# Kernel tuning notes

Measured on AMD Instinct MI355X. Metric: run time of the kernel, lower is better.

Reference implementation:

```python
import jax, jax.numpy as jnp
import numpy as np

EPS = 1e-5

def conv1x1(x, w, b):
    # x: [B,Cin,H,W], w: [Cout,Cin], b: [Cout]
    return jnp.einsum('oi,bihw->bohw', w, x) + b[None, :, None, None]

def self_attention(x, qw, qb, kw, kb, vw, vb, fw, fb):
    B, C, H, W = x.shape
    hid = qw.shape[0]
    q = conv1x1(x, qw, qb).reshape(B, hid, H * W).transpose(0, 2, 1)   # [B,HW,hid]
    k = conv1x1(x, kw, kb).reshape(B, hid, H * W)                      # [B,hid,HW]
    v = conv1x1(x, vw, vb).reshape(B, C, H * W)                        # [B,C,HW]
    attn = jax.nn.softmax(jnp.einsum('bnh,bhm->bnm', q, k), axis=-1)   # [B,HW,HW]
    z = jnp.einsum('bnm,bcm->bnc', attn, v)                            # [B,HW,C]
    # faithful to torch .view(B,C,H,W) on contiguous [B,HW,C]: raw reshape, no transpose
    z = z.reshape(B, C, H, W)
    return conv1x1(z * x, fw, fb) + x

def group_norm_per_channel(y, gw, gb):
    # GroupNorm(num_groups == num_channels): per-channel instance norm, biased var
    mean = y.mean(axis=(2, 3), keepdims=True)
    var = ((y - mean) ** 2).mean(axis=(2, 3), keepdims=True)
    yn = (y - mean) * jax.lax.rsqrt(var + EPS)
    return yn * gw[None, :, None, None] + gb[None, :, None, None]

def setup_inputs() -> dict:
    key = jax.random.key(0)
    ks = jax.random.split(key, 32)
    B, C, H, W = 4, 64, 64, 64
    hid, att = 64, 64
    d = {}
    d['x'] = jax.random.normal(ks[0], (B, C, H, W), jnp.float32)
    d['h'] = jax.random.normal(ks[1], (B, hid, H, W), jnp.float32)
    d['c'] = jax.random.normal(ks[2], (B, hid, H, W), jnp.float32)
    i = 3
    for pre, cin in (('ax', C), ('ah', hid)):
        for nm, cout in (('q', att), ('k', att), ('v', cin), ('f', cin)):
            d[f'{pre}_{nm}w'] = jax.random.normal(ks[i], (cout, cin), jnp.float32) * 0.05; i += 1
            d[f'{pre}_{nm}b'] = jax.random.normal(ks[i], (cout,), jnp.float32) * 0.05; i += 1
    d['conv_w'] = jax.random.normal(ks[i], (4 * hid, C + hid, 3, 3), jnp.float32) * 0.05; i += 1
    d['conv_b'] = jax.random.normal(ks[i], (4 * hid,), jnp.float32) * 0.05; i += 1
    d['gn_w'] = jnp.ones((4 * hid,), jnp.float32)
    d['gn_b'] = jnp.zeros((4 * hid,), jnp.float32)
    return d

def reference(x, h, c,
              ax_qw, ax_qb, ax_kw, ax_kb, ax_vw, ax_vb, ax_fw, ax_fb,
              ah_qw, ah_qb, ah_kw, ah_kb, ah_vw, ah_vb, ah_fw, ah_fb,
              conv_w, conv_b, gn_w, gn_b):
    hid = h.shape[1]
    xa = self_attention(x, ax_qw, ax_qb, ax_kw, ax_kb, ax_vw, ax_vb, ax_fw, ax_fb)
    ha = self_attention(h, ah_qw, ah_qb, ah_kw, ah_kb, ah_vw, ah_vb, ah_fw, ah_fb)
    combined = jnp.concatenate([xa, ha], axis=1)
    y = jax.lax.conv_general_dilated(
        combined, conv_w, window_strides=(1, 1), padding=[(1, 1), (1, 1)],
        dimension_numbers=('NCHW', 'OIHW', 'NCHW')) + conv_b[None, :, None, None]
    y = group_norm_per_channel(y, gn_w, gn_b)
    i, f, o, g = jnp.split(y, 4, axis=1)
    i = jax.nn.sigmoid(i); f = jax.nn.sigmoid(f); o = jax.nn.sigmoid(o); g = jnp.tanh(g)
    c_next = f * c + i * g
    h_next = o * jnp.tanh(c_next)
    return jnp.stack([h_next, c_next])  # [2,B,hid,H,W]
```

## Files before the change

kernel.cpp:

```cpp
#include <hip/hip_runtime.h>
#include <hip/hip_bf16.h>


typedef __hip_bfloat16 bf16;
typedef const __hip_bfloat16* bfp;
typedef short bf16x8 __attribute__((ext_vector_type(8)));
typedef short short4v __attribute__((ext_vector_type(4)));
typedef float f32x4 __attribute__((ext_vector_type(4)));

#define SM_SHIFT 12.0f

__device__ __forceinline__ float ldf(const void* p, long i, int f32) {
    return f32 ? ((const float*)p)[i]
               : __bfloat162float(((const bf16*)p)[i]);
}
__device__ __forceinline__ short f2bf(float f) {
    bf16 h = __float2bfloat16(f);
    return *reinterpret_cast<short*>(&h);
}

__global__ void sniff_kernel(const void* __restrict__ x, int* __restrict__ flag)
{
    const unsigned short* u = (const unsigned short*)x;
    int lane = threadIdx.x;
    int ok = 0;
    for (int i = 0; i < 4; ++i) {
        int e = (u[lane * 4 + i] >> 7) & 0xFF;
        ok += (e >= 100 && e <= 141);
    }
    ok += __shfl_xor(ok, 1, 64);
    ok += __shfl_xor(ok, 2, 64);
    ok += __shfl_xor(ok, 4, 64);
    ok += __shfl_xor(ok, 8, 64);
    ok += __shfl_xor(ok, 16, 64);
    ok += __shfl_xor(ok, 32, 64);
    if (lane == 0) *flag = (ok < 200) ? 1 : 0;
}

__global__ __launch_bounds__(256) void wt_kernel(
    const void* __restrict__ cw, bf16* __restrict__ Wt,
    float* __restrict__ gacc, const int* __restrict__ flag)
{
    if (blockIdx.x == 0) {
        for (int j = 0; j < 8; ++j)
            gacc[threadIdx.x * 8 + j] = 0.f;
    }
    int f32 = *flag;
    int idx = blockIdx.x * 256 + threadIdx.x;
    int tap = idx >> 15;
    int rem = idx & 32767;
    int oc = rem >> 7, ic = rem & 127;
    Wt[idx] = __float2bfloat16(ldf(cw, ((long)oc * 128 + ic) * 9 + tap, f32));
}

__global__ __launch_bounds__(256) void qkv_kernel(
    const void* __restrict__ Xx, const void* __restrict__ Xh,
    const void* __restrict__ qwx, const void* __restrict__ qbx,
    const void* __restrict__ kwx, const void* __restrict__ kbx,
    const void* __restrict__ vwx, const void* __restrict__ vbx,
    const void* __restrict__ qwh, const void* __restrict__ qbh,
    const void* __restrict__ kwh, const void* __restrict__ kbh,
    const void* __restrict__ vwh, const void* __restrict__ vbh,
    bf16* __restrict__ Qx, bf16* __restrict__ Kx, bf16* __restrict__ Vtx,
    bf16* __restrict__ Qh, bf16* __restrict__ Kh, bf16* __restrict__ Vth,
    const int* __restrict__ flag)
{
    __shared__ __align__(16) short xt[64][72];
    __shared__ __align__(16) short wq[64][72];
    __shared__ __align__(16) short wk[64][72];
    __shared__ __align__(16) short wv[64][72];
    int ab  = blockIdx.x >> 8;
    int idx = blockIdx.x & 255;
    int b = idx >> 6;
    int n0 = (idx & 63) * 64;
    int tid = threadIdx.x;
    int wave = tid >> 6, lane = tid & 63;
    int q = lane >> 4, l15 = lane & 15;
    int f32 = *flag;

    const void* X = ab ? Xh : Xx;
    const void* qw = ab ? qwh : qwx; const void* qb = ab ? qbh : qbx;
    const void* kw = ab ? kwh : kwx; const void* kb = ab ? kbh : kbx;
    const void* vw = ab ? vwh : vwx; const void* vb = ab ? vbh : vbx;
    short* Qg  = (short*)(ab ? Qh  : Qx)  + (long)b * 262144;
    short* Kg  = (short*)(ab ? Kh  : Kx)  + (long)b * 262144;
    short* Vtg = (short*)(ab ? Vth : Vtx) + (long)b * 262144;

    if (!f32) {
        const short* q16 = (const short*)qw;
        const short* k16 = (const short*)kw;
        const short* v16 = (const short*)vw;
        for (int rep = 0; rep < 2; ++rep) {
            int j8 = (rep * 256 + tid) * 8;
            *(bf16x8*)&wq[j8 >> 6][j8 & 63] = *(const bf16x8*)(q16 + j8);
            *(bf16x8*)&wk[j8 >> 6][j8 & 63] = *(const bf16x8*)(k16 + j8);
            *(bf16x8*)&wv[j8 >> 6][j8 & 63] = *(const bf16x8*)(v16 + j8);
        }
    } else {
        for (int rep = 0; rep < 16; ++rep) {
            int j = rep * 256 + tid;
            int i = j >> 6, cc = j & 63;
            wq[i][cc] = f2bf(((const float*)qw)[j]);
            wk[i][cc] = f2bf(((const float*)kw)[j]);
            wv[i][cc] = f2bf(((const float*)vw)[j]);
        }
    }
    long xbase = (long)b * 262144;
    for (int rep = 0; rep < 16; ++rep) {
        int c = rep * 4 + (tid >> 6);
        int p = tid & 63;
        xt[p][c] = f2bf(ldf(X, xbase + (long)c * 4096 + n0 + p, f32));
    }
    __syncthreads();

    bf16x8 a0 = *(const bf16x8*)&xt[wave * 16 + l15][q * 8];
    bf16x8 a1 = *(const bf16x8*)&xt[wave * 16 + l15][32 + q * 8];

    for (int ct = 0; ct < 4; ++ct) {
        bf16x8 bq0 = *(const bf16x8*)&wq[ct * 16 + l15][q * 8];
        bf16x8 bq1 = *(const bf16x8*)&wq[ct * 16 + l15][32 + q * 8];
        f32x4 z = (f32x4){0.f, 0.f, 0.f, 0.f};
        z = __builtin_amdgcn_mfma_f32_16x16x32_bf16(a0, bq0, z, 0, 0, 0);
        z = __builtin_amdgcn_mfma_f32_16x16x32_bf16(a1, bq1, z, 0, 0, 0);
        float bias = ldf(qb, ct * 16 + l15, f32);
        for (int reg = 0; reg < 4; ++reg)
            Qg[(long)(n0 + wave * 16 + q * 4 + reg) * 64 + ct * 16 + l15] =
                f2bf(z[reg] + bias);
    }
    for (int ct = 0; ct < 4; ++ct) {
        bf16x8 bk0 = *(const bf16x8*)&wk[ct * 16 + l15][q * 8];
        bf16x8 bk1 = *(const bf16x8*)&wk[ct * 16 + l15][32 + q * 8];
        f32x4 z = (f32x4){0.f, 0.f, 0.f, 0.f};
        z = __builtin_amdgcn_mfma_f32_16x16x32_bf16(a0, bk0, z, 0, 0, 0);
        z = __builtin_amdgcn_mfma_f32_16x16x32_bf16(a1, bk1, z, 0, 0, 0);
        float bias = ldf(kb, ct * 16 + l15, f32);
        for (int reg = 0; reg < 4; ++reg)
            Kg[(long)(n0 + wave * 16 + q * 4 + reg) * 64 + ct * 16 + l15] =
                f2bf(z[reg] + bias);
    }
    bf16x8 av0 = *(const bf16x8*)&wv[wave * 16 + l15][q * 8];
    bf16x8 av1 = *(const bf16x8*)&wv[wave * 16 + l15][32 + q * 8];
    for (int ct = 0; ct < 4; ++ct) {
        bf16x8 bx0 = *(const bf16x8*)&xt[ct * 16 + l15][q * 8];
        bf16x8 bx1 = *(const bf16x8*)&xt[ct * 16 + l15][32 + q * 8];
        f32x4 z = (f32x4){0.f, 0.f, 0.f, 0.f};
        z = __builtin_amdgcn_mfma_f32_16x16x32_bf16(av0, bx0, z, 0, 0, 0);
        z = __builtin_amdgcn_mfma_f32_16x16x32_bf16(av1, bx1, z, 0, 0, 0);
        for (int reg = 0; reg < 4; ++reg) {
            int c_out = wave * 16 + q * 4 + reg;
            float bias = ldf(vb, c_out, f32);
            Vtg[(long)c_out * 4096 + n0 + ct * 16 + l15] = f2bf(z[reg] + bias);
        }
    }
}

__global__ __launch_bounds__(256, 2) void attn_kernel(
    bfp Qx, bfp Kx, bfp Vtx, bf16* Ox,
    bfp Qh, bfp Kh, bfp Vth, bf16* Oh)
{
    __shared__ __align__(16) short ks [2][64][64];
    __shared__ __align__(16) short vts[2][64][64];
    __shared__ __align__(16) short ps[4][16][64];
    int tid = threadIdx.x;
    int wave = tid >> 6, lane = tid & 63;
    int q = lane >> 4, l15 = lane & 15;
    int ab  = blockIdx.x >> 8;
    int idx = blockIdx.x & 255;
    int b = idx >> 6;
    int rt = idx & 63;
    int n0 = rt * 64 + wave * 16;
    const short* Qb  = (const short*)(ab ? Qh  : Qx)  + (long)b * 262144;
    const short* Kb  = (const short*)(ab ? Kh  : Kx)  + (long)b * 262144;
    const short* Vtb = (const short*)(ab ? Vth : Vtx) + (long)b * 262144;
    short* Ob = (short*)(ab ? Oh : Ox) + (long)b * 262144;

    bf16x8 aq0 = *(const bf16x8*)(Qb + (long)(n0 + l15) * 64 + q * 8);
    bf16x8 aq1 = *(const bf16x8*)(Qb + (long)(n0 + l15) * 64 + 32 + q * 8);

    f32x4 acc_o[4];
    for (int ct = 0; ct < 4; ++ct) acc_o[ct] = (f32x4){0.f, 0.f, 0.f, 0.f};
    float l_part[4] = {0.f, 0.f, 0.f, 0.f};

    int swp = (l15 >> 1) & 7;
    int c0 = (q ^ swp) << 3;
    int c1 = ((q + 4) ^ swp) << 3;
    int sw_s = (tid >> 4) & 7;
    int cs = (((tid & 7) ^ sw_s)) << 3;

    int r0 = tid >> 3, r1 = r0 + 32;
    bf16x8 pk0 = *(const bf16x8*)(Kb + (long)r0 * 64 + (tid & 7) * 8);
    bf16x8 pk1 = *(const bf16x8*)(Kb + (long)r1 * 64 + (tid & 7) * 8);
    bf16x8 pv0 = *(const bf16x8*)(Vtb + (long)r0 * 4096 + (tid & 7) * 8);
    bf16x8 pv1 = *(const bf16x8*)(Vtb + (long)r1 * 4096 + (tid & 7) * 8);

    for (int it = 0; it < 64; ++it) {
        int buf = it & 1;
        *(bf16x8*)&ks[buf][r0][cs]  = pk0;
        *(bf16x8*)&ks[buf][r1][cs]  = pk1;
        *(bf16x8*)&vts[buf][r0][cs] = pv0;
        *(bf16x8*)&vts[buf][r1][cs] = pv1;
        __syncthreads();
        if (it + 1 < 64) {
            long m = (long)(it + 1) * 64;
            pk0 = *(const bf16x8*)(Kb + (m + r0) * 64 + (tid & 7) * 8);
            pk1 = *(const bf16x8*)(Kb + (m + r1) * 64 + (tid & 7) * 8);
            pv0 = *(const bf16x8*)(Vtb + (long)r0 * 4096 + m + (tid & 7) * 8);
            pv1 = *(const bf16x8*)(Vtb + (long)r1 * 4096 + m + (tid & 7) * 8);
        }

        f32x4 s[4];
        for (int t = 0; t < 4; ++t) {
            const short* krow = &ks[buf][t * 16 + l15][0];
            bf16x8 bk0 = *(const bf16x8*)(krow + c0);
            bf16x8 bk1 = *(const bf16x8*)(krow + c1);
            f32x4 z = (f32x4){0.f, 0.f, 0.f, 0.f};
            z    = __builtin_amdgcn_mfma_f32_16x16x32_bf16(aq0, bk0, z, 0, 0, 0);
            s[t] = __builtin_amdgcn_mfma_f32_16x16x32_bf16(aq1, bk1, z, 0, 0, 0);
        }

        for (int t = 0; t < 4; ++t) {
            int chunkbase = t << 1 | (l15 >> 3);
            for (int reg = 0; reg < 4; ++reg) {
                float p = __expf(fminf(s[t][reg] - SM_SHIFT, 60.f));
                l_part[reg] += p;
                int n = q * 4 + reg;
                int swn = (n >> 1) & 7;
                ps[wave][n][((chunkbase ^ swn) << 3) | (l15 & 7)] = f2bf(p);
            }
        }

        const short* prow = &ps[wave][l15][0];
        bf16x8 bp0 = *(const bf16x8*)(prow + c0);
        bf16x8 bp1 = *(const bf16x8*)(prow + c1);
        for (int ct = 0; ct < 4; ++ct) {
            const short* vrow = &vts[buf][ct * 16 + l15][0];
            bf16x8 av0 = *(const bf16x8*)(vrow + c0);
            bf16x8 av1 = *(const bf16x8*)(vrow + c1);
            acc_o[ct] = __builtin_amdgcn_mfma_f32_16x16x32_bf16(av0, bp0, acc_o[ct], 0, 0, 0);
            acc_o[ct] = __builtin_amdgcn_mfma_f32_16x16x32_bf16(av1, bp1, acc_o[ct], 0, 0, 0);
        }
    }

    for (int reg = 0; reg < 4; ++reg) {
        l_part[reg] += __shfl_xor(l_part[reg], 1, 64);
        l_part[reg] += __shfl_xor(l_part[reg], 2, 64);
        l_part[reg] += __shfl_xor(l_part[reg], 4, 64);
        l_part[reg] += __shfl_xor(l_part[reg], 8, 64);
    }
    int src = (l15 >> 2) << 4;
    float L0 = __shfl(l_part[0], src, 64);
    float L1 = __shfl(l_part[1], src, 64);
    float L2 = __shfl(l_part[2], src, 64);
    float L3 = __shfl(l_part[3], src, 64);
    int r3 = l15 & 3;
    float ln = (r3 == 0) ? L0 : (r3 == 1) ? L1 : (r3 == 2) ? L2 : L3;
    float iln = 1.f / ln;
    for (int ct = 0; ct < 4; ++ct) {
        short o0 = f2bf(acc_o[ct][0] * iln);
        short o1 = f2bf(acc_o[ct][1] * iln);
        short o2 = f2bf(acc_o[ct][2] * iln);
        short o3 = f2bf(acc_o[ct][3] * iln);
        short* dst = Ob + (long)(n0 + l15) * 64 + ct * 16 + q * 4;
        dst[0] = o0; dst[1] = o1; dst[2] = o2; dst[3] = o3;
    }
}

__global__ __launch_bounds__(256) void attnout_kernel(
    bfp Ox, const void* __restrict__ Xx,
    const void* __restrict__ fwx, const void* __restrict__ fbx,
    bf16* __restrict__ outx,
    bfp Oh, const void* __restrict__ Xh,
    const void* __restrict__ fwh, const void* __restrict__ fbh,
    bf16* __restrict__ outh,
    const int* __restrict__ flag)
{
    __shared__ __align__(16) short fwt[64][72];
    __shared__ __align__(16) short at [64][72];
    int f32 = *flag;
    int ab  = blockIdx.x >> 8;
    int idx = blockIdx.x & 255;
    int b = idx >> 6;
    int h = idx & 63;
    int tid = threadIdx.x;
    int wave = tid >> 6, lane = tid & 63;
    int q = lane >> 4, l15 = lane & 15;
    bfp O = ab ? Oh : Ox;
    const void* X = ab ? Xh : Xx;
    const void* fw = ab ? fwh : fwx;
    const void* fb = ab ? fbh : fbx;
    bf16* out = ab ? outh : outx;

    if (!f32) {
        const short* f16p = (const short*)fw;
        for (int rep = 0; rep < 2; ++rep) {
            int j8 = (rep * 256 + tid) * 8;
            *(bf16x8*)&fwt[j8 >> 6][j8 & 63] = *(const bf16x8*)(f16p + j8);
        }
    } else {
        for (int rep = 0; rep < 16; ++rep) {
            int j = rep * 256 + tid;
            fwt[j >> 6][j & 63] = f2bf(((const float*)fw)[j]);
        }
    }
    const bf16* Ob = O + (long)b * 262144;
    long xbase = (long)b * 262144;
    {
        int w = tid & 63;
        for (int rep = 0; rep < 16; ++rep) {
            int cn = rep * 4 + (tid >> 6);
            float prod = __bfloat162float(Ob[(cn * 64 + h) * 64 + w]) *
                         ldf(X, xbase + (long)cn * 4096 + h * 64 + w, f32);
            at[w][cn] = f2bf(prod);
        }
    }
    __syncthreads();
    bf16x8 a0 = *(const bf16x8*)&fwt[wave * 16 + l15][q * 8];
    bf16x8 a1 = *(const bf16x8*)&fwt[wave * 16 + l15][32 + q * 8];
    short* outp = (short*)out;
    for (int nt = 0; nt < 4; ++nt) {
        bf16x8 b0 = *(const bf16x8*)&at[nt * 16 + l15][q * 8];
        bf16x8 b1 = *(const bf16x8*)&at[nt * 16 + l15][32 + q * 8];
        f32x4 z = (f32x4){0.f, 0.f, 0.f, 0.f};
        z = __builtin_amdgcn_mfma_f32_16x16x32_bf16(a0, b0, z, 0, 0, 0);
        z = __builtin_amdgcn_mfma_f32_16x16x32_bf16(a1, b1, z, 0, 0, 0);
        int w = nt * 16 + l15;
        short4v o4;
        for (int reg = 0; reg < 4; ++reg) {
            int o = wave * 16 + q * 4 + reg;
            float v = z[reg] + ldf(fb, o, f32) +
                      ldf(X, xbase + (long)o * 4096 + h * 64 + w, f32);
            o4[reg] = f2bf(v);
        }
        *(short4v*)(outp + (((long)(b * 64 + h) * 64 + w) * 64 + wave * 16 + q * 4)) = o4;
    }
}

__global__ __launch_bounds__(256) void conv3x3_kernel(
    bfp xa, bfp ha, bfp Wt, const void* __restrict__ cb,
    bf16* __restrict__ y, float* __restrict__ gacc,
    const int* __restrict__ flag)
{
    __shared__ __align__(16) short in_s[3][66][136];
    int f32 = *flag;
    int b = blockIdx.x >> 6;
    int h = blockIdx.x & 63;
    int tid = threadIdx.x;
    int wave = tid >> 6, lane = tid & 63;
    int q = lane >> 4, l15 = lane & 15;

    const short* xab = (const short*)xa + (long)b * 262144;
    const short* hab = (const short*)ha + (long)b * 262144;
    const bf16x8 zv = {0, 0, 0, 0, 0, 0, 0, 0};
    for (int r = 0; r < 3; ++r) {
        int gy = h + r - 1;
        bool valid = (gy >= 0) && (gy < 64);
        for (int s = 0; s < 2; ++s) {
            int strip = s * 256 + tid;
            int w = strip >> 3;
            int c8 = (strip & 7) * 8;
            bf16x8 vx = zv, vh = zv;
            if (valid) {
                vx = *(const bf16x8*)(xab + ((long)gy * 64 + w) * 64 + c8);
                vh = *(const bf16x8*)(hab + ((long)gy * 64 + w) * 64 + c8);
            }
            *(bf16x8*)&in_s[r][w + 1][c8]      = vx;
            *(bf16x8*)&in_s[r][w + 1][64 + c8] = vh;
        }
    }
    if (tid < 96) {
        int r = tid / 32;
        int rest = tid % 32;
        int col = (rest & 1) ? 65 : 0;
        int c8 = (rest >> 1) * 8;
        *(bf16x8*)&in_s[r][col][c8] = zv;
    }
    __syncthreads();

    int oc0 = wave * 64;
    f32x4 acc[4][4];
    for (int mt = 0; mt < 4; ++mt)
        for (int nt = 0; nt < 4; ++nt)
            acc[mt][nt] = (f32x4){0.f, 0.f, 0.f, 0.f};

    const short* Wb = (const short*)Wt;
    for (int tap = 0; tap < 9; ++tap) {
        int dy = tap / 3, dx = tap - dy * 3;
        for (int kc = 0; kc < 4; ++kc) {
            bf16x8 afrag[4];
            for (int mt = 0; mt < 4; ++mt)
                afrag[mt] = *(const bf16x8*)(
                    Wb + ((long)tap * 256 + oc0 + mt * 16 + l15) * 128 + kc * 32 + q * 8);
            for (int nt = 0; nt < 4; ++nt) {
                bf16x8 bfrag = *(const bf16x8*)&in_s[dy][nt * 16 + l15 + dx][kc * 32 + q * 8];
                for (int mt = 0; mt < 4; ++mt)
                    acc[mt][nt] = __builtin_amdgcn_mfma_f32_16x16x32_bf16(
                        afrag[mt], bfrag, acc[mt][nt], 0, 0, 0);
            }
        }
    }

    long ybase = (long)b * 1048576 + (long)h * 64;
    for (int mt = 0; mt < 4; ++mt) {
        for (int reg = 0; reg < 4; ++reg) {
            int oc = oc0 + mt * 16 + q * 4 + reg;
            float bias = ldf(cb, oc, f32);
            float s = 0.f, s2 = 0.f;
            for (int nt = 0; nt < 4; ++nt) {
                float v = acc[mt][nt][reg] + bias;
                ((short*)y)[ybase + (long)oc * 4096 + nt * 16 + l15] = f2bf(v);
                s += v; s2 = fmaf(v, v, s2);
            }
            s  += __shfl_xor(s,  1, 64);  s2 += __shfl_xor(s2, 1, 64);
            s  += __shfl_xor(s,  2, 64);  s2 += __shfl_xor(s2, 2, 64);
            s  += __shfl_xor(s,  4, 64);  s2 += __shfl_xor(s2, 4, 64);
            s  += __shfl_xor(s,  8, 64);  s2 += __shfl_xor(s2, 8, 64);
            if (l15 == 0) {
                atomicAdd(&gacc[b * 256 + oc], s);
                atomicAdd(&gacc[1024 + b * 256 + oc], s2);
            }
        }
    }
}

__global__ __launch_bounds__(256) void gates_kernel(
    bfp y, const float* __restrict__ gacc,
    const void* __restrict__ gw, const void* __restrict__ gb,
    const void* __restrict__ c_in, void* __restrict__ out,
    const int* __restrict__ flag)
{
    int f32 = *flag;
    int idx = blockIdx.x * 256 + threadIdx.x;
    int b = idx >> 18;
    int r = idx & 262143;
    int ch = r >> 12;
    int pix = r & 4095;
    long ybase = (long)b * 1048576;
    float vals[4];
    for (int g = 0; g < 4; ++g) {
        int cc = g * 64 + ch;
        float mu  = gacc[b * 256 + cc] * (1.f / 4096.f);
        float var = gacc[1024 + b * 256 + cc] * (1.f / 4096.f) - mu * mu;
        float rstd = rsqrtf(fmaxf(var, 0.f) + 1e-5f);
        float v = __bfloat162float(y[ybase + (long)cc * 4096 + pix]);
        v = (v - mu) * rstd * ldf(gw, cc, f32) + ldf(gb, cc, f32);
        vals[g] = v;
    }
    float ig = 1.f / (1.f + __expf(-vals[0]));
    float fg = 1.f / (1.f + __expf(-vals[1]));
    float og = 1.f / (1.f + __expf(-vals[2]));
    float gg = tanhf(vals[3]);
    float cprev = ldf(c_in, idx, f32);
    float cn = fg * cprev + ig * gg;
    float hn = og * tanhf(cn);
    if (f32) {
        float* o32 = (float*)out;
        o32[idx] = hn;
        o32[1048576 + idx] = cn;
    } else {
        bf16* o16 = (bf16*)out;
        o16[idx] = __float2bfloat16(hn);
        o16[1048576 + idx] = __float2bfloat16(cn);
    }
}

extern "C" void kernel_launch(void* const* d_in, const int* in_sizes, int n_in,
                              void* d_out, int out_size, void* d_ws, size_t ws_size,
                              hipStream_t stream)
{
    const void* x = d_in[0]; const void* h = d_in[1]; const void* c = d_in[2];
    const void* ax_qw = d_in[3],  *ax_qb = d_in[4];
    const void* ax_kw = d_in[5],  *ax_kb = d_in[6];
    const void* ax_vw = d_in[7],  *ax_vb = d_in[8];
    const void* ax_fw = d_in[9],  *ax_fb = d_in[10];
    const void* ah_qw = d_in[11], *ah_qb = d_in[12];
    const void* ah_kw = d_in[13], *ah_kb = d_in[14];
    const void* ah_vw = d_in[15], *ah_vb = d_in[16];
    const void* ah_fw = d_in[17], *ah_fb = d_in[18];
    const void* conv_w = d_in[19], *conv_b = d_in[20];
    const void* gn_w = d_in[21],  *gn_b = d_in[22];

    char* wsb = (char*)d_ws;
    auto S = [&](int i) { return wsb + ((unsigned long)i << 21); };
    bool fused = ws_size >= (18ul << 20) + 16384;

    bf16* ha = (bf16*)S(0);
    bf16* Wt = (bf16*)S(1);
    bf16 *Qx, *Kx, *Vtx, *Qh, *Kh, *Vth, *xa, *y;
    char* tail;
    if (fused) {
        Qx = (bf16*)S(2); Kx = (bf16*)S(3); Vtx = (bf16*)S(4);
        Qh = (bf16*)S(5); Kh = (bf16*)S(6); Vth = (bf16*)S(7);
        xa = (bf16*)S(8); y = Qx;
        tail = S(9);
    } else {
        Qx = (bf16*)S(2); Kx = (bf16*)S(3); Vtx = (bf16*)S(4);
        Qh = Qx; Kh = Kx; Vth = Vtx;
        xa = (bf16*)S(6); y = Qx;
        tail = S(7);
    }
    bf16* Ox = Qx;
    bf16* Oh = Qh;
    int*  flag = (int*)tail;
    float* gacc = (float*)(tail + 256);

    sniff_kernel<<<1, 64, 0, stream>>>(x, flag);

    if (fused) {
        qkv_kernel<<<512, 256, 0, stream>>>(
            x, h,
            ax_qw, ax_qb, ax_kw, ax_kb, ax_vw, ax_vb,
            ah_qw, ah_qb, ah_kw, ah_kb, ah_vw, ah_vb,
            Qx, Kx, Vtx, Qh, Kh, Vth, flag);
        attn_kernel<<<512, 256, 0, stream>>>(Qx, Kx, Vtx, Ox, Qh, Kh, Vth, Oh);
        attnout_kernel<<<512, 256, 0, stream>>>(
            Ox, x, ax_fw, ax_fb, xa, Oh, h, ah_fw, ah_fb, ha, flag);
    } else {
        qkv_kernel<<<256, 256, 0, stream>>>(
            x, x,
            ax_qw, ax_qb, ax_kw, ax_kb, ax_vw, ax_vb,
            ax_qw, ax_qb, ax_kw, ax_kb, ax_vw, ax_vb,
            Qx, Kx, Vtx, Qx, Kx, Vtx, flag);
        attn_kernel<<<256, 256, 0, stream>>>(Qx, Kx, Vtx, Ox, Qx, Kx, Vtx, Ox);
        attnout_kernel<<<256, 256, 0, stream>>>(
            Ox, x, ax_fw, ax_fb, xa, Ox, x, ax_fw, ax_fb, xa, flag);
        qkv_kernel<<<256, 256, 0, stream>>>(
            h, h,
            ah_qw, ah_qb, ah_kw, ah_kb, ah_vw, ah_vb,
            ah_qw, ah_qb, ah_kw, ah_kb, ah_vw, ah_vb,
            Qh, Kh, Vth, Qh, Kh, Vth, flag);
        attn_kernel<<<256, 256, 0, stream>>>(Qh, Kh, Vth, Oh, Qh, Kh, Vth, Oh);
        attnout_kernel<<<256, 256, 0, stream>>>(
            Oh, h, ah_fw, ah_fb, ha, Oh, h, ah_fw, ah_fb, ha, flag);
    }
    wt_kernel<<<1152, 256, 0, stream>>>(conv_w, Wt, gacc, flag);
    conv3x3_kernel<<<256, 256, 0, stream>>>(xa, ha, Wt, conv_b, y, gacc, flag);
    gates_kernel<<<4096, 256, 0, stream>>>(y, gacc, gn_w, gn_b, c, d_out, flag);
}
```

Measured before the change: 244.0 us.

## Split attention key dimension in two halves and combine partials in attnout

Attention blocks now process only half of the key/value sequence each, doubling the grid from 512 to 1024 blocks to fill more of the CUs. Each half writes unnormalized bf16 partial outputs and per-row softmax sums to workspace. The attnout kernel adds the two partials and normalizes them, which is possible because the softmax uses a fixed shift. This costs extra partial-output traffic, rounds the partials to bf16 before they are summed, and only runs when the workspace is at least 27 MB.

Result: no change. 239.4 us (-1.9%).

```diff
diff --git a/kernel.cpp b/kernel.cpp
--- a/kernel.cpp
+++ b/kernel.cpp
@@ -156,7 +156,8 @@
 
 __global__ __launch_bounds__(256, 2) void attn_kernel(
     bfp Qx, bfp Kx, bfp Vtx, bf16* Ox,
-    bfp Qh, bfp Kh, bfp Vth, bf16* Oh)
+    bfp Qh, bfp Kh, bfp Vth, bf16* Oh,
+    float* __restrict__ lw, int split)
 {
     __shared__ __align__(16) short ks [2][64][64];
     __shared__ __align__(16) short vts[2][64][64];
@@ -164,15 +165,21 @@
     int tid = threadIdx.x;
     int wave = tid >> 6, lane = tid & 63;
     int q = lane >> 4, l15 = lane & 15;
-    int ab  = blockIdx.x >> 8;
     int idx = blockIdx.x & 255;
+    int ab, half, mstart, ntile;
+    if (split) {
+        ab = blockIdx.x >> 9; half = (blockIdx.x >> 8) & 1;
+        mstart = half * 2048; ntile = 32;
+    } else {
+        ab = blockIdx.x >> 8; half = 0; mstart = 0; ntile = 64;
+    }
     int b = idx >> 6;
     int rt = idx & 63;
     int n0 = rt * 64 + wave * 16;
     const short* Qb  = (const short*)(ab ? Qh  : Qx)  + (long)b * 262144;
     const short* Kb  = (const short*)(ab ? Kh  : Kx)  + (long)b * 262144;
     const short* Vtb = (const short*)(ab ? Vth : Vtx) + (long)b * 262144;
-    short* Ob = (short*)(ab ? Oh : Ox) + (long)b * 262144;
+    short* Ob = (short*)(ab ? Oh : Ox) + (long)half * (1l << 20) + (long)b * 262144;
 
     bf16x8 aq0 = *(const bf16x8*)(Qb + (long)(n0 + l15) * 64 + q * 8);
     bf16x8 aq1 = *(const bf16x8*)(Qb + (long)(n0 + l15) * 64 + 32 + q * 8);
@@ -188,20 +195,20 @@
     int cs = (((tid & 7) ^ sw_s)) << 3;
 
     int r0 = tid >> 3, r1 = r0 + 32;
-    bf16x8 pk0 = *(const bf16x8*)(Kb + (long)r0 * 64 + (tid & 7) * 8);
-    bf16x8 pk1 = *(const bf16x8*)(Kb + (long)r1 * 64 + (tid & 7) * 8);
-    bf16x8 pv0 = *(const bf16x8*)(Vtb + (long)r0 * 4096 + (tid & 7) * 8);
-    bf16x8 pv1 = *(const bf16x8*)(Vtb + (long)r1 * 4096 + (tid & 7) * 8);
-
-    for (int it = 0; it < 64; ++it) {
+    bf16x8 pk0 = *(const bf16x8*)(Kb + (long)(mstart + r0) * 64 + (tid & 7) * 8);
+    bf16x8 pk1 = *(const bf16x8*)(Kb + (long)(mstart + r1) * 64 + (tid & 7) * 8);
+    bf16x8 pv0 = *(const bf16x8*)(Vtb + (long)r0 * 4096 + mstart + (tid & 7) * 8);
+    bf16x8 pv1 = *(const bf16x8*)(Vtb + (long)r1 * 4096 + mstart + (tid & 7) * 8);
+
+    for (int it = 0; it < ntile; ++it) {
         int buf = it & 1;
         *(bf16x8*)&ks[buf][r0][cs]  = pk0;
         *(bf16x8*)&ks[buf][r1][cs]  = pk1;
         *(bf16x8*)&vts[buf][r0][cs] = pv0;
         *(bf16x8*)&vts[buf][r1][cs] = pv1;
         __syncthreads();
-        if (it + 1 < 64) {
-            long m = (long)(it + 1) * 64;
+        if (it + 1 < ntile) {
+            long m = (long)mstart + (long)(it + 1) * 64;
             pk0 = *(const bf16x8*)(Kb + (m + r0) * 64 + (tid & 7) * 8);
             pk1 = *(const bf16x8*)(Kb + (m + r1) * 64 + (tid & 7) * 8);
             pv0 = *(const bf16x8*)(Vtb + (long)r0 * 4096 + m + (tid & 7) * 8);
@@ -247,21 +254,36 @@
         l_part[reg] += __shfl_xor(l_part[reg], 4, 64);
         l_part[reg] += __shfl_xor(l_part[reg], 8, 64);
     }
-    int src = (l15 >> 2) << 4;
-    float L0 = __shfl(l_part[0], src, 64);
-    float L1 = __shfl(l_part[1], src, 64);
-    float L2 = __shfl(l_part[2], src, 64);
-    float L3 = __shfl(l_part[3], src, 64);
-    int r3 = l15 & 3;
-    float ln = (r3 == 0) ? L0 : (r3 == 1) ? L1 : (r3 == 2) ? L2 : L3;
-    float iln = 1.f / ln;
-    for (int ct = 0; ct < 4; ++ct) {
-        short o0 = f2bf(acc_o[ct][0] * iln);
-        short o1 = f2bf(acc_o[ct][1] * iln);
-        short o2 = f2bf(acc_o[ct][2] * iln);
-        short o3 = f2bf(acc_o[ct][3] * iln);
-        short* dst = Ob + (long)(n0 + l15) * 64 + ct * 16 + q * 4;
-        dst[0] = o0; dst[1] = o1; dst[2] = o2; dst[3] = o3;
+    if (split) {
+        if (l15 == 0) {
+            float* lp = lw + (long)ab * 32768 + (long)half * 16384
+                           + (long)b * 4096 + n0 + q * 4;
+            lp[0] = l_part[0]; lp[1] = l_part[1];
+            lp[2] = l_part[2]; lp[3] = l_part[3];
+        }
+        for (int ct = 0; ct < 4; ++ct) {
+            short* dst = Ob + (long)(n0 + l15) * 64 + ct * 16 + q * 4;
+            dst[0] = f2bf(acc_o[ct][0]);
+            dst[1] = f2bf(acc_o[ct][1]);
+            dst[2] = f2bf(acc_o[ct][2]);
+            dst[3] = f2bf(acc_o[ct][3]);
+        }
+    } else {
+        int src = (l15 >> 2) << 4;
+        float L0 = __shfl(l_part[0], src, 64);
+        float L1 = __shfl(l_part[1], src, 64);
+        float L2 = __shfl(l_part[2], src, 64);
+        float L3 = __shfl(l_part[3], src, 64);
+        int r3 = l15 & 3;
+        float ln = (r3 == 0) ? L0 : (r3 == 1) ? L1 : (r3 == 2) ? L2 : L3;
+        float iln = 1.f / ln;
+        for (int ct = 0; ct < 4; ++ct) {
+            short* dst = Ob + (long)(n0 + l15) * 64 + ct * 16 + q * 4;
+            dst[0] = f2bf(acc_o[ct][0] * iln);
+            dst[1] = f2bf(acc_o[ct][1] * iln);
+            dst[2] = f2bf(acc_o[ct][2] * iln);
+            dst[3] = f2bf(acc_o[ct][3] * iln);
+        }
     }
 }
 
@@ -272,6 +294,7 @@
     bfp Oh, const void* __restrict__ Xh,
     const void* __restrict__ fwh, const void* __restrict__ fbh,
     bf16* __restrict__ outh,
+    const float* __restrict__ lw, int split,
     const int* __restrict__ flag)
 {
     __shared__ __align__(16) short fwt[64][72];
@@ -302,14 +325,25 @@
             fwt[j >> 6][j & 63] = f2bf(((const float*)fw)[j]);
         }
     }
-    const bf16* Ob = O + (long)b * 262144;
+    const bf16* Ob0 = O + (long)b * 262144;
+    const bf16* Ob1 = Ob0 + (1l << 20);
+    const float* lp0 = lw + (long)ab * 32768 + (long)b * 4096;
+    const float* lp1 = lp0 + 16384;
     long xbase = (long)b * 262144;
     {
         int w = tid & 63;
         for (int rep = 0; rep < 16; ++rep) {
             int cn = rep * 4 + (tid >> 6);
-            float prod = __bfloat162float(Ob[(cn * 64 + h) * 64 + w]) *
-                         ldf(X, xbase + (long)cn * 4096 + h * 64 + w, f32);
+            int n = cn * 64 + h;
+            float o;
+            if (split) {
+                float iln = 1.f / (lp0[n] + lp1[n]);
+                o = (__bfloat162float(Ob0[(long)n * 64 + w]) +
+                     __bfloat162float(Ob1[(long)n * 64 + w])) * iln;
+            } else {
+                o = __bfloat162float(Ob0[(long)n * 64 + w]);
+            }
+            float prod = o * ldf(X, xbase + (long)cn * 4096 + h * 64 + w, f32);
             at[w][cn] = f2bf(prod);
         }
     }
@@ -481,27 +515,35 @@
 
     char* wsb = (char*)d_ws;
     auto S = [&](int i) { return wsb + ((unsigned long)i << 21); };
-    bool fused = ws_size >= (18ul << 20) + 16384;
+    bool splitm = ws_size >= (27ul << 20);
+    bool fused  = splitm || ws_size >= (18ul << 20) + 16384;
 
     bf16* ha = (bf16*)S(0);
     bf16* Wt = (bf16*)S(1);
-    bf16 *Qx, *Kx, *Vtx, *Qh, *Kh, *Vth, *xa, *y;
+    bf16 *Qx, *Kx, *Vtx, *Qh, *Kh, *Vth, *xa, *y, *Ox, *Oh;
     char* tail;
-    if (fused) {
+    if (splitm) {
         Qx = (bf16*)S(2); Kx = (bf16*)S(3); Vtx = (bf16*)S(4);
         Qh = (bf16*)S(5); Kh = (bf16*)S(6); Vth = (bf16*)S(7);
-        xa = (bf16*)S(8); y = Qx;
+        xa = (bf16*)S(8);
+        Ox = (bf16*)S(9);
+        Oh = (bf16*)S(11);
+        y = Qx;
+        tail = S(13);
+    } else if (fused) {
+        Qx = (bf16*)S(2); Kx = (bf16*)S(3); Vtx = (bf16*)S(4);
+        Qh = (bf16*)S(5); Kh = (bf16*)S(6); Vth = (bf16*)S(7);
+        xa = (bf16*)S(8); Ox = Qx; Oh = Qh; y = Qx;
         tail = S(9);
     } else {
         Qx = (bf16*)S(2); Kx = (bf16*)S(3); Vtx = (bf16*)S(4);
         Qh = Qx; Kh = Kx; Vth = Vtx;
-        xa = (bf16*)S(6); y = Qx;
+        xa = (bf16*)S(6); Ox = Qx; Oh = Qh; y = Qx;
         tail = S(7);
     }
-    bf16* Ox = Qx;
-    bf16* Oh = Qh;
     int*  flag = (int*)tail;
     float* gacc = (float*)(tail + 256);
+    float* lw   = (float*)(tail + 256 + 8192);
 
     sniff_kernel<<<1, 64, 0, stream>>>(x, flag);
 
@@ -511,26 +553,36 @@
             ax_qw, ax_qb, ax_kw, ax_kb, ax_vw, ax_vb,
             ah_qw, ah_qb, ah_kw, ah_kb, ah_vw, ah_vb,
             Qx, Kx, Vtx, Qh, Kh, Vth, flag);
-        attn_kernel<<<512, 256, 0, stream>>>(Qx, Kx, Vtx, Ox, Qh, Kh, Vth, Oh);
-        attnout_kernel<<<512, 256, 0, stream>>>(
-            Ox, x, ax_fw, ax_fb, xa, Oh, h, ah_fw, ah_fb, ha, flag);
+        if (splitm) {
+            attn_kernel<<<1024, 256, 0, stream>>>(
+                Qx, Kx, Vtx, Ox, Qh, Kh, Vth, Oh, lw, 1);
+            attnout_kernel<<<512, 256, 0, stream>>>(
+                Ox, x, ax_fw, ax_fb, xa, Oh, h, ah_fw, ah_fb, ha, lw, 1, flag);
+        } else {
+            attn_kernel<<<512, 256, 0, stream>>>(
+                Qx, Kx, Vtx, Ox, Qh, Kh, Vth, Oh, lw, 0);
+            attnout_kernel<<<512, 256, 0, stream>>>(
+                Ox, x, ax_fw, ax_fb, xa, Oh, h, ah_fw, ah_fb, ha, lw, 0, flag);
+        }
     } else {
         qkv_kernel<<<256, 256, 0, stream>>>(
             x, x,
             ax_qw, ax_qb, ax_kw, ax_kb, ax_vw, ax_vb,
             ax_qw, ax_qb, ax_kw, ax_kb, ax_vw, ax_vb,
             Qx, Kx, Vtx, Qx, Kx, Vtx, flag);
-        attn_kernel<<<256, 256, 0, stream>>>(Qx, Kx, Vtx, Ox, Qx, Kx, Vtx, Ox);
+        attn_kernel<<<256, 256, 0, stream>>>(
+            Qx, Kx, Vtx, Ox, Qx, Kx, Vtx, Ox, lw, 0);
         attnout_kernel<<<256, 256, 0, stream>>>(
-            Ox, x, ax_fw, ax_fb, xa, Ox, x, ax_fw, ax_fb, xa, flag);
+            Ox, x, ax_fw, ax_fb, xa, Ox, x, ax_fw, ax_fb, xa, lw, 0, flag);
         qkv_kernel<<<256, 256, 0, stream>>>(
             h, h,
             ah_qw, ah_qb, ah_kw, ah_kb, ah_vw, ah_vb,
             ah_qw, ah_qb, ah_kw, ah_kb, ah_vw, ah_vb,
             Qh, Kh, Vth, Qh, Kh, Vth, flag);
-        attn_kernel<<<256, 256, 0, stream>>>(Qh, Kh, Vth, Oh, Qh, Kh, Vth, Oh);
+        attn_kernel<<<256, 256, 0, stream>>>(
+            Qh, Kh, Vth, Oh, Qh, Kh, Vth, Oh, lw, 0);
         attnout_kernel<<<256, 256, 0, stream>>>(
-            Oh, h, ah_fw, ah_fb, ha, Oh, h, ah_fw, ah_fb, ha, flag);
+            Oh, h, ah_fw, ah_fb, ha, Oh, h, ah_fw, ah_fb, ha, lw, 0, flag);
     }
     wt_kernel<<<1152, 256, 0, stream>>>(conv_w, Wt, gacc, flag);
     conv3x3_kernel<<<256, 256, 0, stream>>>(xa, ha, Wt, conv_b, y, gacc, flag);
```
